# Optimization experiments

Hardware: AMD Instinct MI355X
Metric: run time of the kernel (lower is better)

## Reference

```python
import jax, jax.numpy as jnp
import numpy as np

B = 4096; CPG = 2; NPC = 25              # graphs, components/graph, nodes/component
N = B * CPG * NPC; C = B * CPG; E = 409600
IN_CH = 128; HID = 256; L = 3; S = 64; M = 8; NCLS = 2
BN_EPS = 1e-5

def _leaky(x):
    return jax.nn.leaky_relu(x, 0.01)

def _gin_conv(x, src, dst, wa, ba, wb, bb):
    # GINConv with eps=0: mlp(x + sum_{j in N(i)} x_j); messages flow src->dst
    agg = jnp.zeros_like(x).at[dst].add(x[src])
    h = x + agg
    return jax.nn.relu(h @ wa + ba) @ wb + bb

def setup_inputs():
    key = jax.random.key(0)
    ks = jax.random.split(key, 12)
    rn = lambda k, shp: jax.random.normal(k, shp, jnp.float32) * 0.05
    return {
        "x": jax.random.normal(ks[0], (N, IN_CH), jnp.float32),
        "w0a": rn(ks[1], (IN_CH, HID)), "b0a": jnp.zeros((HID,), jnp.float32),
        "w0b": rn(ks[2], (HID, HID)), "b0b": jnp.zeros((HID,), jnp.float32),
        "wra": rn(ks[3], (L - 1, HID, HID)), "bra": jnp.zeros((L - 1, HID), jnp.float32),
        "wrb": rn(ks[4], (L - 1, HID, HID)), "brb": jnp.zeros((L - 1, HID), jnp.float32),
        "Wc": jax.random.uniform(ks[5], (HID, S * M), jnp.float32, -1.0, 1.0),
        "fc1_w": rn(ks[6], (S, 32)), "fc1_b": jnp.zeros((32,), jnp.float32),
        "bn_g": jnp.ones((32,), jnp.float32), "bn_b": jnp.zeros((32,), jnp.float32),
        "fc2_w": rn(ks[7], (32, NCLS)), "fc2_b": jnp.zeros((NCLS,), jnp.float32),
        "edge_index": jax.random.randint(ks[8], (2, E), 0, N, jnp.int32),
        "node2comp": (jnp.arange(N, dtype=jnp.int32) // NPC),
        "comp2graph": (jnp.arange(C, dtype=jnp.int32) // CPG),
        "comp_pos": (jnp.arange(C, dtype=jnp.int32) % CPG),
        "n_graphs": B,
        "max_comps": CPG,
    }

def reference(x, w0a, b0a, w0b, b0b, wra, bra, wrb, brb, Wc, fc1_w, fc1_b, bn_g, bn_b, fc2_w, fc2_b, edge_index, node2comp, comp2graph, comp_pos, n_graphs, max_comps):
    src, dst = edge_index[0], edge_index[1]
    # --- GIN backbone (num_layers convs, ReLU between layers) ---
    h = _gin_conv(x, src, dst, w0a, b0a, w0b, b0b)
    for i in range(wra.shape[0]):
        h = jax.nn.relu(h)
        h = _gin_conv(h, src, dst, wra[i], bra[i], wrb[i], brb[i])
    # --- per-connected-component mean pooling ---
    n_comp = comp2graph.shape[0]
    comp_sum = jax.ops.segment_sum(h, node2comp, num_segments=n_comp)           # [C, d]
    comp_size = jax.ops.segment_sum(jnp.ones((h.shape[0],), h.dtype), node2comp, num_segments=n_comp)
    # torch.mean over the zero-padded cardinality dim divides by the per-graph MAX component size
    graph_maxc = jax.ops.segment_max(comp_size, comp2graph, num_segments=n_graphs)
    comp_mean = comp_sum / graph_maxc[comp2graph][:, None]
    # --- pad components into [B, max_comps, d] ---
    X = jnp.zeros((n_graphs, max_comps, h.shape[1]), h.dtype).at[comp2graph, comp_pos].set(comp_mean)
    # --- set-rep classifier ---
    t = _leaky(jnp.einsum('bcd,dk->bck', X, Wc))                                # [B, maxC, S*M]
    s = fc1_w.shape[0]; m = Wc.shape[1] // s
    t = t.reshape(t.shape[0], t.shape[1], m, s)                                 # view(B, maxC, n_elements, n_hidden_sets)
    t = jnp.max(t, axis=2)
    t = jnp.sum(t, axis=1)                                                      # [B, S]
    t = t @ fc1_w + fc1_b
    mu = jnp.mean(t, axis=0); var = jnp.var(t, axis=0)                          # BN, batch stats (track_running_stats=False)
    t = (t - mu) / jnp.sqrt(var + BN_EPS) * bn_g + bn_b
    t = _leaky(t)
    out = t @ fc2_w + fc2_b
    return jax.nn.log_softmax(out, axis=1)
```

## Files before the change

### kernel.cpp

```cpp
#include <hip/hip_runtime.h>
#include <hip/hip_fp16.h>
#include <math.h>

typedef unsigned short u16;
typedef float f32x4 __attribute__((ext_vector_type(4)));
typedef __bf16 bf16x8 __attribute__((ext_vector_type(8)));

__device__ __forceinline__ float b2f(u16 u) {
    union { unsigned int i; float f; } v; v.i = ((unsigned int)u) << 16; return v.f;
}
__device__ __forceinline__ u16 f2b(float f) {
    union { float f; unsigned int i; } v; v.f = f;
    unsigned int lsb = (v.i >> 16) & 1u;
    return (u16)((v.i + 0x7fffu + lsb) >> 16);
}

__global__ __launch_bounds__(256)
void k_count(const int* __restrict__ dst, int* __restrict__ cnt, int E)
{
    int e = blockIdx.x * 256 + threadIdx.x;
    if (e < E) atomicAdd(&cnt[dst[e]], 1);
}

__global__ __launch_bounds__(256)
void k_scan1(const int* __restrict__ cnt, int* __restrict__ rowptr,
             int* __restrict__ bsum, int N)
{
    __shared__ int s[256];
    int t = threadIdx.x, i = blockIdx.x * 256 + t;
    int v = (i < N) ? cnt[i] : 0;
    s[t] = v;
    __syncthreads();
#pragma unroll
    for (int off = 1; off < 256; off <<= 1) {
        int add = (t >= off) ? s[t - off] : 0;
        __syncthreads();
        s[t] += add;
        __syncthreads();
    }
    if (i < N) rowptr[i] = s[t] - v;
    if (t == 255) bsum[blockIdx.x] = s[255];
}

__global__ __launch_bounds__(256)
void k_scan2(const int* __restrict__ bsum, int* __restrict__ bscan, int nb)
{
    __shared__ int s[256];
    int t = threadIdx.x;
    int g[4], e[4];
    int base = t * 4;
#pragma unroll
    for (int j = 0; j < 4; ++j) g[j] = (base + j < nb) ? bsum[base + j] : 0;
    e[0] = 0; e[1] = g[0]; e[2] = g[0] + g[1]; e[3] = g[0] + g[1] + g[2];
    int tsum = e[3] + g[3];
    s[t] = tsum;
    __syncthreads();
#pragma unroll
    for (int off = 1; off < 256; off <<= 1) {
        int add = (t >= off) ? s[t - off] : 0;
        __syncthreads();
        s[t] += add;
        __syncthreads();
    }
    int texcl = s[t] - tsum;
#pragma unroll
    for (int j = 0; j < 4; ++j)
        if (base + j < nb) bscan[base + j] = texcl + e[j];
}

__global__ __launch_bounds__(256)
void k_scan3(int* __restrict__ rowptr, const int* __restrict__ bscan,
             int* __restrict__ cursor, int N)
{
    int i = blockIdx.x * 256 + threadIdx.x;
    if (i >= N) return;
    int r = rowptr[i] + bscan[i >> 8];
    rowptr[i] = r;
    cursor[i] = r;
}

__global__ __launch_bounds__(256)
void k_fill(const int* __restrict__ src, const int* __restrict__ dst,
            int* __restrict__ cursor, int* __restrict__ col, int E)
{
    int e = blockIdx.x * 256 + threadIdx.x;
    if (e >= E) return;
    int pos = atomicAdd(&cursor[dst[e]], 1);
    col[pos] = src[e];
}

__global__ void k_T(const float* __restrict__ in, u16* __restrict__ out, int K, int N)
{
    int t = blockIdx.x * 256 + threadIdx.x;
    if (t >= K * N) return;
    int n = t / K, k = t % K;
    out[t] = f2b(in[k * N + n]);
}

#define CCAP 512

template<int K, bool RELU, bool F32SRC>
__global__ __launch_bounds__(512, 6)
void k_gin(const void* __restrict__ hsrc,
           const int* __restrict__ cnt, const int* __restrict__ rowptr,
           const int* __restrict__ col,
           const u16* __restrict__ WaT, const float* __restrict__ ba,
           const u16* __restrict__ WbT, const float* __restrict__ bb,
           u16* __restrict__ Hout, int Ntot, int Etot)
{
    __shared__ u16 AH[64 * 256];
    __shared__ int colLDS[CCAP];

    const int tid = threadIdx.x, lane = tid & 63, wave = tid >> 6;
    const int bm0 = blockIdx.x * 64;
    const int lc = lane & 15, lr = (lane >> 4) * 4;
    const int cw0 = wave * 32;
    const int l15 = lane & 15, lq = lane >> 4;

    const int rp0 = rowptr[bm0];
    const int rpE = (bm0 + 64 < Ntot) ? rowptr[bm0 + 64] : Etot;
    const int total = rpE - rp0;
    for (int i = tid; i < total && i < CCAP; i += 512) colLDS[i] = col[rp0 + i];

    bf16x8 bpre0 = *(const bf16x8*)(WaT + (size_t)(cw0 + l15) * K + lq * 8);
    bf16x8 bpre1 = *(const bf16x8*)(WaT + (size_t)(cw0 + 16 + l15) * K + lq * 8);
    __syncthreads();

    {
        constexpr int NSEG = K / 8;
        const int gr = tid >> 3, gseg = tid & 7;
        const int node = bm0 + gr;
        const int nn = cnt[node], rp = rowptr[node];
        const int jbase = rp - rp0;
        const int nIt = nn + 1;

        float acc[NSEG];
#pragma unroll
        for (int i = 0; i < NSEG; ++i) acc[i] = 0.f;

        if (F32SRC) {
            const float4* bp = (const float4*)hsrc;
            const int stride = K / 4, off = gseg * (NSEG / 4);
            const float4* p = bp + (size_t)node * stride + off;
            float4 a0 = p[0], a1 = p[1];
            for (int t = 0; t < nIt; ++t) {
                float4 b0 = p[2], b1 = p[3];
                int tn = (t + 1 < nIt) ? t + 1 : t;
                int jl = jbase + tn - 1;
                int idxN = (tn == 0) ? node : ((jl < CCAP) ? colLDS[jl] : col[rp + tn - 1]);
                const float4* q = bp + (size_t)idxN * stride + off;
                float4 n0 = q[0], n1 = q[1];
                if (RELU) {
                    acc[0] += fmaxf(a0.x,0.f); acc[1] += fmaxf(a0.y,0.f); acc[2] += fmaxf(a0.z,0.f); acc[3] += fmaxf(a0.w,0.f);
                    acc[4] += fmaxf(a1.x,0.f); acc[5] += fmaxf(a1.y,0.f); acc[6] += fmaxf(a1.z,0.f); acc[7] += fmaxf(a1.w,0.f);
                    acc[8] += fmaxf(b0.x,0.f); acc[9] += fmaxf(b0.y,0.f); acc[10]+= fmaxf(b0.z,0.f); acc[11]+= fmaxf(b0.w,0.f);
                    acc[12]+= fmaxf(b1.x,0.f); acc[13]+= fmaxf(b1.y,0.f); acc[14]+= fmaxf(b1.z,0.f); acc[15]+= fmaxf(b1.w,0.f);
                } else {
                    acc[0] += a0.x; acc[1] += a0.y; acc[2] += a0.z; acc[3] += a0.w;
                    acc[4] += a1.x; acc[5] += a1.y; acc[6] += a1.z; acc[7] += a1.w;
                    acc[8] += b0.x; acc[9] += b0.y; acc[10]+= b0.z; acc[11]+= b0.w;
                    acc[12]+= b1.x; acc[13]+= b1.y; acc[14]+= b1.z; acc[15]+= b1.w;
                }
                a0 = n0; a1 = n1; p = q;
            }
        } else {
            const uint4* bp = (const uint4*)hsrc;
            const int stride = K / 8, off = gseg * (NSEG / 8);
            const uint4* p = bp + (size_t)node * stride + off;
            uint4 a0 = p[0], a1 = p[1];
            for (int t = 0; t < nIt; ++t) {
                uint4 b0 = p[2], b1 = p[3];
                int tn = (t + 1 < nIt) ? t + 1 : t;
                int jl = jbase + tn - 1;
                int idxN = (tn == 0) ? node : ((jl < CCAP) ? colLDS[jl] : col[rp + tn - 1]);
                const uint4* q = bp + (size_t)idxN * stride + off;
                uint4 n0 = q[0], n1 = q[1];
                u16 vs[32] __attribute__((aligned(16)));
                *(uint4*)(vs + 0)  = a0; *(uint4*)(vs + 8)  = a1;
                *(uint4*)(vs + 16) = b0; *(uint4*)(vs + 24) = b1;
#pragma unroll
                for (int i2 = 0; i2 < 32; ++i2) {
                    float x = b2f(vs[i2]);
                    acc[i2] += RELU ? fmaxf(x, 0.f) : x;
                }
                a0 = n0; a1 = n1; p = q;
            }
        }

        const int k0 = gseg * NSEG;
        constexpr int NKC = NSEG / 8;
        u16* const rbase = AH + (gr >> 4) * 512 + (gr & 15) * 8;
#pragma unroll
        for (int cc = 0; cc < NKC; ++cc) {
            const int k = k0 + cc * 8;
            u16 tmp[8] __attribute__((aligned(16)));
#pragma unroll
            for (int jj = 0; jj < 8; ++jj) tmp[jj] = f2b(acc[cc * 8 + jj]);
            *(uint4*)(rbase + (k >> 5) * 2048 + ((k >> 3) & 3) * 128) = *(const uint4*)tmp;
        }
    }
    __syncthreads();

    constexpr int NK1 = K / 32;
    f32x4 acc1[4][2];
#pragma unroll
    for (int r = 0; r < 4; ++r)
#pragma unroll
        for (int c = 0; c < 2; ++c) acc1[r][c] = (f32x4){0.f, 0.f, 0.f, 0.f};

#pragma unroll
    for (int kb = 0; kb < NK1; ++kb) {
        bf16x8 a[4], b[2];
        if (kb == 0) { b[0] = bpre0; b[1] = bpre1; }
        else {
#pragma unroll
            for (int c = 0; c < 2; ++c)
                b[c] = *(const bf16x8*)(WaT + (size_t)(cw0 + c * 16 + l15) * K + kb * 32 + lq * 8);
        }
#pragma unroll
        for (int r = 0; r < 4; ++r)
            a[r] = *(const bf16x8*)&AH[(kb * 256 + r * 64 + lane) * 8];
        __builtin_amdgcn_s_setprio(1);
#pragma unroll
        for (int r = 0; r < 4; ++r)
#pragma unroll
            for (int c = 0; c < 2; ++c)
                acc1[r][c] = __builtin_amdgcn_mfma_f32_16x16x32_bf16(a[r], b[c], acc1[r][c], 0, 0, 0);
        __builtin_amdgcn_s_setprio(0);
    }
    __syncthreads();

#pragma unroll
    for (int c = 0; c < 2; ++c) {
        const int n = cw0 + c * 16 + lc;
        const float bv = ba[n];
        const int nb = (n >> 5) * 256 + ((n >> 3) & 3) * 16;
#pragma unroll
        for (int r = 0; r < 4; ++r)
#pragma unroll
            for (int i = 0; i < 4; ++i)
                AH[(nb + r * 64 + lr + i) * 8 + (n & 7)] = f2b(fmaxf(acc1[r][c][i] + bv, 0.f));
    }
    __syncthreads();

    f32x4 acc2[4][2];
#pragma unroll
    for (int r = 0; r < 4; ++r)
#pragma unroll
        for (int c = 0; c < 2; ++c) acc2[r][c] = (f32x4){0.f, 0.f, 0.f, 0.f};

#pragma unroll
    for (int kb = 0; kb < 8; ++kb) {
        bf16x8 a[4], b[2];
#pragma unroll
        for (int c = 0; c < 2; ++c)
            b[c] = *(const bf16x8*)(WbT + (size_t)(cw0 + c * 16 + l15) * 256 + kb * 32 + lq * 8);
#pragma unroll
        for (int r = 0; r < 4; ++r)
            a[r] = *(const bf16x8*)&AH[(kb * 256 + r * 64 + lane) * 8];
        __builtin_amdgcn_s_setprio(1);
#pragma unroll
        for (int r = 0; r < 4; ++r)
#pragma unroll
            for (int c = 0; c < 2; ++c)
                acc2[r][c] = __builtin_amdgcn_mfma_f32_16x16x32_bf16(a[r], b[c], acc2[r][c], 0, 0, 0);
        __builtin_amdgcn_s_setprio(0);
    }
#pragma unroll
    for (int c = 0; c < 2; ++c) {
        const int n = cw0 + c * 16 + lc;
        const float bv = bb[n];
#pragma unroll
        for (int r = 0; r < 4; ++r)
#pragma unroll
            for (int i = 0; i < 4; ++i)
                Hout[(size_t)(bm0 + r * 16 + lr + i) * 256 + n] = f2b(acc2[r][c][i] + bv);
    }
}

__global__ __launch_bounds__(256)
void k_lin(const u16* __restrict__ A, const u16* __restrict__ WT,
           float* __restrict__ C)
{
    __shared__ u16 As[64 * 40];
    __shared__ u16 Bs[256 * 40];
    const int tid = threadIdx.x, lane = tid & 63, wave = tid >> 6;
    const int bm0 = blockIdx.x * 64, bn0 = blockIdx.y * 256;
    const int fm = lane & 15, fk = (lane >> 4) * 8;
    const int lc = lane & 15, lr = (lane >> 4) * 4;
    const int cw0 = wave * 64;
    const int sr = tid >> 2, sc = tid & 3;

    f32x4 acc[4][4];
#pragma unroll
    for (int r = 0; r < 4; ++r)
#pragma unroll
        for (int c = 0; c < 4; ++c) acc[r][c] = (f32x4){0.f, 0.f, 0.f, 0.f};

    for (int k0 = 0; k0 < 256; k0 += 32) {
        *(uint4*)&As[sr * 40 + sc * 8] =
            *(const uint4*)(A + (size_t)(bm0 + sr) * 256 + k0 + sc * 8);
        {
            const uint4* wp = (const uint4*)(WT + (size_t)(bn0 + tid) * 256 + k0);
#pragma unroll
            for (int c = 0; c < 4; ++c)
                *(uint4*)&Bs[tid * 40 + c * 8] = wp[c];
        }
        __syncthreads();
        bf16x8 a[4], b[4];
#pragma unroll
        for (int r = 0; r < 4; ++r) a[r] = *(const bf16x8*)&As[(r * 16 + fm) * 40 + fk];
#pragma unroll
        for (int c = 0; c < 4; ++c) b[c] = *(const bf16x8*)&Bs[(cw0 + c * 16 + fm) * 40 + fk];
#pragma unroll
        for (int r = 0; r < 4; ++r)
#pragma unroll
            for (int c = 0; c < 4; ++c)
                acc[r][c] = __builtin_amdgcn_mfma_f32_16x16x32_bf16(a[r], b[c], acc[r][c], 0, 0, 0);
        __syncthreads();
    }
#pragma unroll
    for (int c = 0; c < 4; ++c) {
        const int col = bn0 + cw0 + c * 16 + lc;
#pragma unroll
        for (int r = 0; r < 4; ++r)
#pragma unroll
            for (int i = 0; i < 4; ++i) {
                float v = acc[r][c][i];
                v = (v >= 0.f) ? v : 0.01f * v;
                C[(size_t)(bm0 + r * 16 + lr + i) * 512 + col] = v;
            }
    }
}

__global__ void k_pool(const u16* __restrict__ H, u16* __restrict__ Xc)
{
    int c = blockIdx.x, f = threadIdx.x;
    const u16* p = H + (size_t)c * 25 * 256 + f;
    float s = 0.f;
#pragma unroll
    for (int j = 0; j < 25; ++j) s += b2f(p[j * 256]);
    Xc[(size_t)c * 256 + f] = f2b(s / 25.0f);
}

__global__ void k_setpool(const float* __restrict__ T, float* __restrict__ Tp)
{
    int tid = blockIdx.x * 256 + threadIdx.x;
    int b = tid >> 6, s = tid & 63;
    float acc = 0.f;
#pragma unroll
    for (int c = 0; c < 2; ++c) {
        const float* row = T + ((size_t)(b * 2 + c)) * 512 + s;
        float mx = row[0];
#pragma unroll
        for (int m = 1; m < 8; ++m) mx = fmaxf(mx, row[m * 64]);
        acc += mx;
    }
    Tp[tid] = acc;
}

__global__ void k_fc1(const float* __restrict__ Tp, const float* __restrict__ w,
                      const float* __restrict__ b, float* __restrict__ T1)
{
    int tid = blockIdx.x * 256 + threadIdx.x;
    int bb = tid >> 5, j = tid & 31;
    float s = b[j];
#pragma unroll
    for (int k = 0; k < 64; ++k) s += Tp[bb * 64 + k] * w[k * 32 + j];
    T1[tid] = s;
}

__global__ void k_bnstats(const float* __restrict__ T1, float* __restrict__ stats)
{
    __shared__ float r1[256], r2[256];
    const int j = blockIdx.x, t = threadIdx.x;
    float s = 0.f, ss = 0.f;
    for (int b = t; b < 4096; b += 256) {
        float v = T1[b * 32 + j];
        s += v; ss += v * v;
    }
    r1[t] = s; r2[t] = ss;
    __syncthreads();
    for (int off = 128; off > 0; off >>= 1) {
        if (t < off) { r1[t] += r1[t + off]; r2[t] += r2[t + off]; }
        __syncthreads();
    }
    if (t == 0) {
        float mu  = r1[0] * (1.f / 4096.f);
        float var = r2[0] * (1.f / 4096.f) - mu * mu;
        stats[j]      = mu;
        stats[32 + j] = 1.f / sqrtf(var + 1e-5f);
    }
}

__global__ void k_head(const float* __restrict__ T1, const float* __restrict__ stats,
                       const float* __restrict__ g, const float* __restrict__ bb,
                       const float* __restrict__ w2, const float* __restrict__ b2,
                       float* __restrict__ out)
{
    const int b = blockIdx.x * 256 + threadIdx.x;
    float l0 = b2[0], l1 = b2[1];
#pragma unroll
    for (int j = 0; j < 32; ++j) {
        float v = (T1[b * 32 + j] - stats[j]) * stats[32 + j] * g[j] + bb[j];
        v = (v >= 0.f) ? v : 0.01f * v;
        l0 += v * w2[j * 2];
        l1 += v * w2[j * 2 + 1];
    }
    float mx  = fmaxf(l0, l1);
    float lse = mx + logf(expf(l0 - mx) + expf(l1 - mx));
    out[b * 2]     = l0 - lse;
    out[b * 2 + 1] = l1 - lse;
}

extern "C" void kernel_launch(void* const* d_in, const int* in_sizes, int n_in,
                              void* d_out, int out_size, void* d_ws, size_t ws_size,
                              hipStream_t stream)
{
    (void)n_in; (void)out_size; (void)ws_size;
    constexpr int NN = 204800, NCOMP = 8192, NGRAPH = 4096;

    const float* x    = (const float*)d_in[0];
    const float* w0a  = (const float*)d_in[1];
    const float* b0a  = (const float*)d_in[2];
    const float* w0b  = (const float*)d_in[3];
    const float* b0b  = (const float*)d_in[4];
    const float* wra  = (const float*)d_in[5];
    const float* bra  = (const float*)d_in[6];
    const float* wrb  = (const float*)d_in[7];
    const float* brb  = (const float*)d_in[8];
    const float* Wc   = (const float*)d_in[9];
    const float* f1w  = (const float*)d_in[10];
    const float* f1b  = (const float*)d_in[11];
    const float* bng  = (const float*)d_in[12];
    const float* bnb  = (const float*)d_in[13];
    const float* f2w  = (const float*)d_in[14];
    const float* f2bb = (const float*)d_in[15];
    const int* ei   = (const int*)d_in[16];
    const int  E    = in_sizes[16] / 2;
    const int* src  = ei;
    const int* dst  = ei + E;

    char* ws = (char*)d_ws;
    u16*    H1  = (u16*)ws;
    u16*    H0  = (u16*)(ws + (size_t)104857600);
    u16*    wt  = (u16*)(ws + (size_t)209715200);
    u16 *WT0 = wt, *WT1 = wt + 65536, *WT2 = wt + 131072, *WT3 = wt + 196608,
        *WT4 = wt + 262144, *WT5 = wt + 327680, *WT6 = wt + 393216;
    char* csr = ws + (size_t)210763776;
    int* cnt    = (int*)csr;
    int* rowptr = (int*)(csr + 819200);
    int* cursor = (int*)(csr + 1638400);
    int* col    = (int*)(csr + 2457600);
    int* bsum   = (int*)(csr + 4096000);
    int* bscan  = (int*)(csr + 4100096);
    u16*   Xc    = (u16*)ws;
    float* Tfull = (float*)(ws + (size_t)16777216);
    float* Tp    = (float*)(ws + (size_t)33554432);
    float* T1    = (float*)(ws + (size_t)41943040);
    float* stats = (float*)(ws + (size_t)46137344);

    const dim3 blk(256);
    const dim3 blk512(512);
    const int NB = NN / 256;

    hipMemsetAsync(cnt, 0, NN * 4, stream);
    k_count<<<(E + 255) / 256, blk, 0, stream>>>(dst, cnt, E);
    k_scan1<<<NB, blk, 0, stream>>>(cnt, rowptr, bsum, NN);
    k_scan2<<<1, blk, 0, stream>>>(bsum, bscan, NB);
    k_scan3<<<NB, blk, 0, stream>>>(rowptr, bscan, cursor, NN);
    k_fill<<<(E + 255) / 256, blk, 0, stream>>>(src, dst, cursor, col, E);

    k_T<<<128, blk, 0, stream>>>(w0a, WT0, 128, 256);
    k_T<<<256, blk, 0, stream>>>(w0b, WT1, 256, 256);
    k_T<<<256, blk, 0, stream>>>(wra,          WT2, 256, 256);
    k_T<<<256, blk, 0, stream>>>(wra + 65536,  WT3, 256, 256);
    k_T<<<256, blk, 0, stream>>>(wrb,          WT4, 256, 256);
    k_T<<<256, blk, 0, stream>>>(wrb + 65536,  WT5, 256, 256);
    k_T<<<512, blk, 0, stream>>>(Wc, WT6, 256, 512);

    k_gin<128, false, true><<<NN / 64, blk512, 0, stream>>>(
        x, cnt, rowptr, col, WT0, b0a, WT1, b0b, H0, NN, E);
    k_gin<256, true, false><<<NN / 64, blk512, 0, stream>>>(
        H0, cnt, rowptr, col, WT2, bra, WT4, brb, H1, NN, E);
    k_gin<256, true, false><<<NN / 64, blk512, 0, stream>>>(
        H1, cnt, rowptr, col, WT3, bra + 256, WT5, brb + 256, H0, NN, E);

    k_pool<<<NCOMP, blk, 0, stream>>>(H0, Xc);
    k_lin<<<dim3(NCOMP / 64, 2), blk, 0, stream>>>(Xc, WT6, Tfull);
    k_setpool<<<(NGRAPH * 64) / 256, blk, 0, stream>>>(Tfull, Tp);
    k_fc1<<<(NGRAPH * 32) / 256, blk, 0, stream>>>(Tp, f1w, f1b, T1);
    k_bnstats<<<32, blk, 0, stream>>>(T1, stats);
    k_head<<<NGRAPH / 256, blk, 0, stream>>>(T1, stats, bng, bnb, f2w, f2bb, (float*)d_out);
}
```

Measured before the change: 694.1 us.

## Swizzle LDS layout, swap MFMA operands for packed bf16 stores, merge setup kernels

The GIN kernel's LDS tile now uses an XOR swizzle. The MFMA operands are swapped so each lane holds four consecutive output columns, which lets the epilogues write packed bf16 pairs through v_cvt_pk_bf16_f32 as vector stores instead of scalar 16-bit stores. The edge-count kernel and the seven weight-transpose launches are merged into one setup kernel to cut launch overhead. This aims to reduce LDS bank conflicts and scattered global stores, but it relies on the swizzle and transposed accumulator layout being consistent across all reads and writes.

```diff
diff --git a/kernel.cpp b/kernel.cpp
--- a/kernel.cpp
+++ b/kernel.cpp
@@ -14,12 +14,10 @@
     unsigned int lsb = (v.i >> 16) & 1u;
     return (u16)((v.i + 0x7fffu + lsb) >> 16);
 }
-
-__global__ __launch_bounds__(256)
-void k_count(const int* __restrict__ dst, int* __restrict__ cnt, int E)
-{
-    int e = blockIdx.x * 256 + threadIdx.x;
-    if (e < E) atomicAdd(&cnt[dst[e]], 1);
+__device__ __forceinline__ unsigned int cvtpk(float lo, float hi) {
+    unsigned int r;
+    asm("v_cvt_pk_bf16_f32 %0, %1, %2" : "=v"(r) : "v"(lo), "v"(hi));
+    return r;
 }
 
 __global__ __launch_bounds__(256)
@@ -89,12 +87,25 @@
     col[pos] = src[e];
 }
 
-__global__ void k_T(const float* __restrict__ in, u16* __restrict__ out, int K, int N)
+__global__ __launch_bounds__(256)
+void k_setup(const float* __restrict__ w0a, const float* __restrict__ w0b,
+             const float* __restrict__ wra, const float* __restrict__ wrb,
+             const float* __restrict__ Wc,  u16* __restrict__ wt,
+             const int* __restrict__ dst, int* __restrict__ cnt, int E)
 {
     int t = blockIdx.x * 256 + threadIdx.x;
-    if (t >= K * N) return;
-    int n = t / K, k = t % K;
-    out[t] = f2b(in[k * N + n]);
+    if (t < E) atomicAdd(&cnt[dst[t]], 1);
+
+    const float* in; u16* out; int K, N, l;
+    if      (t < 32768)  { in = w0a;          out = wt;          K = 128; N = 256; l = t; }
+    else if (t < 98304)  { in = w0b;          out = wt + 65536;  K = 256; N = 256; l = t - 32768; }
+    else if (t < 163840) { in = wra;          out = wt + 131072; K = 256; N = 256; l = t - 98304; }
+    else if (t < 229376) { in = wra + 65536;  out = wt + 196608; K = 256; N = 256; l = t - 163840; }
+    else if (t < 294912) { in = wrb;          out = wt + 262144; K = 256; N = 256; l = t - 229376; }
+    else if (t < 360448) { in = wrb + 65536;  out = wt + 327680; K = 256; N = 256; l = t - 294912; }
+    else if (t < 491520) { in = Wc;           out = wt + 393216; K = 256; N = 512; l = t - 360448; }
+    else return;
+    out[l] = f2b(in[(l % K) * N + l / K]);
 }
 
 #define CCAP 512
@@ -113,7 +124,6 @@
 
     const int tid = threadIdx.x, lane = tid & 63, wave = tid >> 6;
     const int bm0 = blockIdx.x * 64;
-    const int lc = lane & 15, lr = (lane >> 4) * 4;
     const int cw0 = wave * 32;
     const int l15 = lane & 15, lq = lane >> 4;
 
@@ -189,14 +199,17 @@
 
         const int k0 = gseg * NSEG;
         constexpr int NKC = NSEG / 8;
-        u16* const rbase = AH + (gr >> 4) * 512 + (gr & 15) * 8;
 #pragma unroll
         for (int cc = 0; cc < NKC; ++cc) {
             const int k = k0 + cc * 8;
-            u16 tmp[8] __attribute__((aligned(16)));
-#pragma unroll
-            for (int jj = 0; jj < 8; ++jj) tmp[jj] = f2b(acc[cc * 8 + jj]);
-            *(uint4*)(rbase + (k >> 5) * 2048 + ((k >> 3) & 3) * 128) = *(const uint4*)tmp;
+            const int s  = (k >> 5) * 256 + (gr >> 4) * 64 + ((k >> 3) & 3) * 16 + (gr & 15);
+            const int sp = s ^ ((k >> 5) & 7);
+            uint4 pk;
+            pk.x = cvtpk(acc[cc * 8 + 0], acc[cc * 8 + 1]);
+            pk.y = cvtpk(acc[cc * 8 + 2], acc[cc * 8 + 3]);
+            pk.z = cvtpk(acc[cc * 8 + 4], acc[cc * 8 + 5]);
+            pk.w = cvtpk(acc[cc * 8 + 6], acc[cc * 8 + 7]);
+            *(uint4*)(AH + sp * 8) = pk;
         }
     }
     __syncthreads();
@@ -219,27 +232,33 @@
         }
 #pragma unroll
         for (int r = 0; r < 4; ++r)
-            a[r] = *(const bf16x8*)&AH[(kb * 256 + r * 64 + lane) * 8];
+            a[r] = *(const bf16x8*)&AH[(kb * 256 + r * 64 + (lane ^ (kb & 7))) * 8];
         __builtin_amdgcn_s_setprio(1);
 #pragma unroll
         for (int r = 0; r < 4; ++r)
 #pragma unroll
             for (int c = 0; c < 2; ++c)
-                acc1[r][c] = __builtin_amdgcn_mfma_f32_16x16x32_bf16(a[r], b[c], acc1[r][c], 0, 0, 0);
+                acc1[r][c] = __builtin_amdgcn_mfma_f32_16x16x32_bf16(b[c], a[r], acc1[r][c], 0, 0, 0);
         __builtin_amdgcn_s_setprio(0);
     }
     __syncthreads();
 
 #pragma unroll
     for (int c = 0; c < 2; ++c) {
-        const int n = cw0 + c * 16 + lc;
-        const float bv = ba[n];
-        const int nb = (n >> 5) * 256 + ((n >> 3) & 3) * 16;
-#pragma unroll
-        for (int r = 0; r < 4; ++r)
-#pragma unroll
-            for (int i = 0; i < 4; ++i)
-                AH[(nb + r * 64 + lr + i) * 8 + (n & 7)] = f2b(fmaxf(acc1[r][c][i] + bv, 0.f));
+        const int n0 = cw0 + c * 16 + lq * 4;
+        const float4 bv = *(const float4*)(ba + n0);
+        const int sbase = (n0 >> 5) * 256 + ((n0 >> 3) & 3) * 16 + l15;
+        const int sx = (n0 >> 5) & 7;
+#pragma unroll
+        for (int r = 0; r < 4; ++r) {
+            float v0 = fmaxf(acc1[r][c][0] + bv.x, 0.f);
+            float v1 = fmaxf(acc1[r][c][1] + bv.y, 0.f);
+            float v2 = fmaxf(acc1[r][c][2] + bv.z, 0.f);
+            float v3 = fmaxf(acc1[r][c][3] + bv.w, 0.f);
+            uint2 pk; pk.x = cvtpk(v0, v1); pk.y = cvtpk(v2, v3);
+            const int sp = (sbase + r * 64) ^ sx;
+            *(uint2*)(AH + sp * 8 + (n0 & 7)) = pk;
+        }
     }
     __syncthreads();
 
@@ -257,24 +276,27 @@
             b[c] = *(const bf16x8*)(WbT + (size_t)(cw0 + c * 16 + l15) * 256 + kb * 32 + lq * 8);
 #pragma unroll
         for (int r = 0; r < 4; ++r)
-            a[r] = *(const bf16x8*)&AH[(kb * 256 + r * 64 + lane) * 8];
+            a[r] = *(const bf16x8*)&AH[(kb * 256 + r * 64 + (lane ^ (kb & 7))) * 8];
         __builtin_amdgcn_s_setprio(1);
 #pragma unroll
         for (int r = 0; r < 4; ++r)
 #pragma unroll
             for (int c = 0; c < 2; ++c)
-                acc2[r][c] = __builtin_amdgcn_mfma_f32_16x16x32_bf16(a[r], b[c], acc2[r][c], 0, 0, 0);
+                acc2[r][c] = __builtin_amdgcn_mfma_f32_16x16x32_bf16(b[c], a[r], acc2[r][c], 0, 0, 0);
         __builtin_amdgcn_s_setprio(0);
     }
 #pragma unroll
     for (int c = 0; c < 2; ++c) {
-        const int n = cw0 + c * 16 + lc;
-        const float bv = bb[n];
-#pragma unroll
-        for (int r = 0; r < 4; ++r)
-#pragma unroll
-            for (int i = 0; i < 4; ++i)
-                Hout[(size_t)(bm0 + r * 16 + lr + i) * 256 + n] = f2b(acc2[r][c][i] + bv);
+        const int n0 = cw0 + c * 16 + lq * 4;
+        const float4 bv = *(const float4*)(bb + n0);
+#pragma unroll
+        for (int r = 0; r < 4; ++r) {
+            const int node = bm0 + r * 16 + l15;
+            uint2 pk;
+            pk.x = cvtpk(acc2[r][c][0] + bv.x, acc2[r][c][1] + bv.y);
+            pk.y = cvtpk(acc2[r][c][2] + bv.z, acc2[r][c][3] + bv.w);
+            *(uint2*)(Hout + (size_t)node * 256 + n0) = pk;
+        }
     }
 }
 
@@ -465,19 +487,11 @@
     const int NB = NN / 256;
 
     hipMemsetAsync(cnt, 0, NN * 4, stream);
-    k_count<<<(E + 255) / 256, blk, 0, stream>>>(dst, cnt, E);
+    k_setup<<<1920, blk, 0, stream>>>(w0a, w0b, wra, wrb, Wc, wt, dst, cnt, E);
     k_scan1<<<NB, blk, 0, stream>>>(cnt, rowptr, bsum, NN);
     k_scan2<<<1, blk, 0, stream>>>(bsum, bscan, NB);
     k_scan3<<<NB, blk, 0, stream>>>(rowptr, bscan, cursor, NN);
     k_fill<<<(E + 255) / 256, blk, 0, stream>>>(src, dst, cursor, col, E);
-
-    k_T<<<128, blk, 0, stream>>>(w0a, WT0, 128, 256);
-    k_T<<<256, blk, 0, stream>>>(w0b, WT1, 256, 256);
-    k_T<<<256, blk, 0, stream>>>(wra,          WT2, 256, 256);
-    k_T<<<256, blk, 0, stream>>>(wra + 65536,  WT3, 256, 256);
-    k_T<<<256, blk, 0, stream>>>(wrb,          WT4, 256, 256);
-    k_T<<<256, blk, 0, stream>>>(wrb + 65536,  WT5, 256, 256);
-    k_T<<<512, blk, 0, stream>>>(Wc, WT6, 256, 512);
 
     k_gin<128, false, true><<<NN / 64, blk512, 0, stream>>>(
         x, cnt, rowptr, col, WT0, b0a, WT1, b0b, H0, NN, E);
```

New measurement: 723.0 us. 4.2% more time.
